# Kernel optimization log

Hardware: AMD Instinct MI355X
Metric: run time of the kernel (lower is better)

Reference implementation:

```python
import math
import jax, jax.numpy as jnp
import numpy as np

B, L, N, DM, H = 4, 12, 512, 64, 8
D = DM // H
FACTOR = 5  # args.spatial_factor


def setup_inputs() -> dict:
    key = jax.random.key(0)
    ks = jax.random.split(key, 6)
    s = 1.0 / math.sqrt(DM)
    return {
        "queries": jax.random.normal(ks[0], (B, L, N, DM), jnp.float32),
        "keys": jax.random.normal(ks[1], (B, L, N, DM), jnp.float32),
        "values": jax.random.normal(ks[2], (B, L, N, DM), jnp.float32),
        "Wq": jax.random.normal(ks[3], (DM, DM), jnp.float32) * s,
        "bq": jnp.zeros((DM,), jnp.float32),
        "Wk": jax.random.normal(ks[4], (DM, DM), jnp.float32) * s,
        "bk": jnp.zeros((DM,), jnp.float32),
        "Wv": jax.random.normal(ks[5], (DM, DM), jnp.float32) * s,
        "bv": jnp.zeros((DM,), jnp.float32),
    }


def reference(queries, keys, values, Wq, bq, Wk, bk, Wv, bv):
    # QKV projections (torch nn.Linear), then split heads and move to [B,H,N,L,D]
    q = jnp.transpose((queries @ Wq + bq).reshape(B, L, N, H, D), (0, 3, 2, 1, 4))
    k = jnp.transpose((keys @ Wk + bk).reshape(B, L, N, H, D), (0, 3, 2, 1, 4))
    v = jnp.transpose((values @ Wv + bv).reshape(B, L, N, H, D), (0, 3, 2, 1, 4))

    sample_k = min(FACTOR * int(np.ceil(np.log(N))), N)  # = n_top = effect_N

    # --- _prob_QK: random K sampling over the N (spatial) axis ---
    idx = jax.random.randint(jax.random.key(42), (N, sample_k), 0, N)  # [N, sk]
    K_sample = k[:, :, idx]                       # [B,H,N,sk,L,D] gather
    # Q.unsqueeze(-2) @ K_sample^T -> [B,H,N,L,sk], then transposed to [B,H,L,N,sk]
    qk_s = jnp.einsum('bhnld,bhnsld->bhlns', q, K_sample)
    M = qk_s.max(axis=-1) - qk_s.sum(axis=-1) / N  # sparsity measure [B,H,L,N]
    _, M_top = jax.lax.top_k(M, sample_k)          # [B,H,L,n_top]

    q_t = jnp.transpose(q, (0, 1, 3, 2, 4))        # [B,H,L,N,D]
    Q_red = jnp.take_along_axis(q_t, M_top[..., None], axis=3)  # [B,H,L,n_top,D]
    scores = jnp.einsum('bhltd,bhnld->bhltn', Q_red, k) / math.sqrt(D)

    # --- context: mean of V over nodes, overwritten at top queries ---
    attn = jax.nn.softmax(scores, axis=-1)                        # [B,H,L,n_top,N]
    attn_ret = jnp.einsum('bhltn,bhnld->bhltd', attn, v)          # [B,H,L,n_top,D]
    ctx = jnp.broadcast_to(v.mean(axis=2)[:, :, :, None, :], (B, H, L, N, D))
    bi = jnp.arange(B)[:, None, None, None]
    hi = jnp.arange(H)[None, :, None, None]
    li = jnp.arange(L)[None, None, :, None]
    ctx = ctx.at[bi, hi, li, M_top].set(attn_ret)                 # scatter-write

    out = jnp.transpose(ctx, (0, 2, 3, 1, 4)).reshape(B, L, N, DM)
    return out  # dropout p=0.0 -> identity
```

## Files before the change

kernel.cpp:

```cpp
#include <hip/hip_runtime.h>
#include <stdint.h>
#include <math.h>

#define BB 4
#define LL 12
#define NN 512
#define DMM 64
#define HH 8
#define DD 8
#define SK 35
#define IDX_TOTAL (NN*SK)
#define PADK 12

__device__ __forceinline__ void tf2x32(uint32_t k0, uint32_t k1, uint32_t x0, uint32_t x1,
                                       uint32_t& o0, uint32_t& o1) {
  const uint32_t ks2 = k0 ^ k1 ^ 0x1BD11BDAu;
  uint32_t a = x0 + k0, b = x1 + k1;
#define TF_R(r) { a += b; b = (b << (r)) | (b >> (32 - (r))); b ^= a; }
  TF_R(13) TF_R(15) TF_R(26) TF_R(6)
  a += k1;  b += ks2 + 1u;
  TF_R(17) TF_R(29) TF_R(16) TF_R(24)
  a += ks2; b += k0 + 2u;
  TF_R(13) TF_R(15) TF_R(26) TF_R(6)
  a += k0;  b += k1 + 3u;
  TF_R(17) TF_R(29) TF_R(16) TF_R(24)
  a += k1;  b += ks2 + 4u;
  TF_R(13) TF_R(15) TF_R(26) TF_R(6)
  a += ks2; b += k0 + 5u;
#undef TF_R
  o0 = a; o1 = b;
}

__global__ __launch_bounds__(256) void proj_idx_kernel(
    const float* __restrict__ Xq, const float* __restrict__ Xk, const float* __restrict__ Xv,
    const float* __restrict__ Wq_, const float* __restrict__ Wk_, const float* __restrict__ Wv_,
    const float* __restrict__ bq_, const float* __restrict__ bk_, const float* __restrict__ bv_,
    float* __restrict__ Oq, float* __restrict__ Ok, float* __restrict__ Ov,
    int* __restrict__ idxT) {
  const int tz = blockIdx.y;
  if (tz == 3) {
    int gid = blockIdx.x * 256 + threadIdx.x;
    if (gid < IDX_TOTAL) {
      int r = gid & (NN - 1);
      int s = gid >> 9;
      uint32_t ka, kb;
      tf2x32(0u, 42u, 0u, 1u, ka, kb);
      uint32_t b1, b2;
      tf2x32(ka, kb, 0u, (uint32_t)(r * SK + s), b1, b2);
      idxT[gid] = (int)((b1 ^ b2) & (uint32_t)(NN - 1));
    }
    return;
  }
  const float* X    = (tz == 0) ? Xq  : (tz == 1) ? Xk  : Xv;
  const float* W    = (tz == 0) ? Wq_ : (tz == 1) ? Wk_ : Wv_;
  const float* bias = (tz == 0) ? bq_ : (tz == 1) ? bk_ : bv_;
  float* O          = (tz == 0) ? Oq  : (tz == 1) ? Ok  : Ov;

  __shared__ __align__(16) float Ws[64][64];
  __shared__ __align__(16) float Xs[64][68];
  __shared__ float bs[64];

  const int tid = threadIdx.x;
  const size_t rowBase = (size_t)blockIdx.x * 64;
  const float* Xb = X + rowBase * 64;
  #pragma unroll
  for (int i = 0; i < 4; ++i) {
    int idx = tid + i*256;
    ((float4*)Ws)[idx] = ((const float4*)W)[idx];
    int r = idx >> 4, c = (idx & 15) << 2;
    *(float4*)&Xs[r][c] = ((const float4*)Xb)[idx];
  }
  if (tid < 64) bs[tid] = bias[tid];
  __syncthreads();

  const int hcol = tid & 7;
  const int rb   = tid >> 3;
  float4 bv0 = *(float4*)&bs[hcol*8];
  float4 bv1 = *(float4*)&bs[hcol*8+4];
  float acc[2][8];
  #pragma unroll
  for (int i = 0; i < 2; ++i) {
    acc[i][0]=bv0.x; acc[i][1]=bv0.y; acc[i][2]=bv0.z; acc[i][3]=bv0.w;
    acc[i][4]=bv1.x; acc[i][5]=bv1.y; acc[i][6]=bv1.z; acc[i][7]=bv1.w;
  }
  #pragma unroll 8
  for (int m = 0; m < 64; ++m) {
    float4 w0 = *(const float4*)&Ws[m][hcol*8];
    float4 w1 = *(const float4*)&Ws[m][hcol*8+4];
    float x0 = Xs[rb][m];
    float x1 = Xs[rb+32][m];
    acc[0][0]=fmaf(x0,w0.x,acc[0][0]); acc[0][1]=fmaf(x0,w0.y,acc[0][1]);
    acc[0][2]=fmaf(x0,w0.z,acc[0][2]); acc[0][3]=fmaf(x0,w0.w,acc[0][3]);
    acc[0][4]=fmaf(x0,w1.x,acc[0][4]); acc[0][5]=fmaf(x0,w1.y,acc[0][5]);
    acc[0][6]=fmaf(x0,w1.z,acc[0][6]); acc[0][7]=fmaf(x0,w1.w,acc[0][7]);
    acc[1][0]=fmaf(x1,w0.x,acc[1][0]); acc[1][1]=fmaf(x1,w0.y,acc[1][1]);
    acc[1][2]=fmaf(x1,w0.z,acc[1][2]); acc[1][3]=fmaf(x1,w0.w,acc[1][3]);
    acc[1][4]=fmaf(x1,w1.x,acc[1][4]); acc[1][5]=fmaf(x1,w1.y,acc[1][5]);
    acc[1][6]=fmaf(x1,w1.z,acc[1][6]); acc[1][7]=fmaf(x1,w1.w,acc[1][7]);
  }
  #pragma unroll
  for (int i = 0; i < 2; ++i) {
    size_t R = rowBase + rb + 32*i;
    int bI = (int)(R / (LL*NN));
    int lI = (int)((R / NN) % LL);
    int nI = (int)(R % NN);
    size_t off = ((((size_t)bI*HH + hcol)*LL + lI)*NN + nI)*DD;
    *(float4*)&O[off]     = make_float4(acc[i][0],acc[i][1],acc[i][2],acc[i][3]);
    *(float4*)&O[off + 4] = make_float4(acc[i][4],acc[i][5],acc[i][6],acc[i][7]);
  }
}

__global__ __launch_bounds__(256) void mkeys_kernel(
    const float* __restrict__ Qt, const float* __restrict__ Kt,
    const int* __restrict__ idxT, uint32_t* __restrict__ fkW) {
  const int gb = blockIdx.x;
  const int bid = gb >> 1, half = gb & 1;
  const int tid = threadIdx.x;
  __shared__ __align__(16) float Ks[NN][PADK];
  const size_t slabOff = (size_t)bid * (NN*DD);

  const float4* kg = (const float4*)(Kt + slabOff);
  #pragma unroll
  for (int i = 0; i < 2; ++i) {
    int r = tid + i*256;
    float4 a = kg[r*2], c = kg[r*2+1];
    *(float4*)&Ks[r][0] = a; *(float4*)&Ks[r][4] = c;
  }
  const int row = half*256 + tid;
  const float4* qp = (const float4*)(Qt + slabOff + (size_t)row*DD);
  float4 qa = qp[0], qb = qp[1];
  int jv[SK];
  const int* gi = idxT + row;
  #pragma unroll
  for (int s = 0; s < SK; ++s) jv[s] = gi[s*NN];
  __syncthreads();

  float mx = -INFINITY, sm = 0.f;
  #pragma unroll
  for (int s = 0; s < SK; ++s) {
    int j = jv[s];
    float4 c0 = *(const float4*)&Ks[j][0];
    float4 c1 = *(const float4*)&Ks[j][4];
    float dot = qa.x*c0.x + qa.y*c0.y + qa.z*c0.z + qa.w*c0.w
              + qb.x*c1.x + qb.y*c1.y + qb.z*c1.z + qb.w*c1.w;
    mx = fmaxf(mx, dot);
    sm += dot;
  }
  float m = mx - sm * (1.0f/NN);
  uint32_t u = __float_as_uint(m);
  fkW[bid*NN + row] = (u & 0x80000000u) ? ~u : (u | 0x80000000u);
}

__global__ __launch_bounds__(256) void attn2_kernel(
    const float* __restrict__ Qt, const float* __restrict__ Kt,
    const float* __restrict__ Vt, const uint32_t* __restrict__ fkW,
    float* __restrict__ out) {
  const int gb = blockIdx.x;
  const int bid = gb >> 1, half = gb & 1;
  const int l = bid % LL;
  const int h = (bid / LL) % HH;
  const int b = bid / (LL*HH);
  const int tid = threadIdx.x;
  const int wave = tid >> 6, lane = tid & 63;

  __shared__ __align__(16) uint64_t keys[NN];
  __shared__ int sel[256];
  __shared__ int listRow[SK];
  __shared__ int listSlot[SK];
  __shared__ int cnt2;
  __shared__ __align__(16) float attnOut[SK][8];
  __shared__ __align__(16) float redD[4][64][8];
  __shared__ __align__(16) float vm[8];

  const size_t slabOff = (size_t)bid * (NN*DD);

  {
    const uint32_t* fp = fkW + bid*NN;
    uint32_t f0 = fp[tid], f1 = fp[tid + 256];
    keys[tid]       = ((uint64_t)f0 << 32) | (uint32_t)(NN - 1 - tid);
    keys[tid + 256] = ((uint64_t)f1 << 32) | (uint32_t)(NN - 1 - (tid + 256));
  }
  sel[tid] = -1;
  if (tid == 0) cnt2 = 0;
  __syncthreads();

  {
    const int row = half*256 + tid;
    const uint64_t my = keys[row];
    const ulonglong2* kq = (const ulonglong2*)keys;
    int cnt = 0;
    #pragma unroll 8
    for (int jb = 0; jb < NN/2; ++jb) {
      ulonglong2 kv = kq[jb];
      cnt += (kv.x > my) ? 1 : 0;
      cnt += (kv.y > my) ? 1 : 0;
    }
    if (cnt < SK) {
      sel[tid] = cnt;
      int p = atomicAdd(&cnt2, 1);
      listRow[p] = row;
      listSlot[p] = cnt;
    }
  }
  __syncthreads();
  const int C = cnt2;

  const float4* kp = (const float4*)(Kt + slabOff);
  const float4* vp = (const float4*)(Vt + slabOff);

  if (wave == 0) {
    float a[8] = {0,0,0,0,0,0,0,0};
    #pragma unroll
    for (int j = 0; j < 8; ++j) {
      const float4* vr = vp + (size_t)(lane + 64*j)*2;
      float4 v0 = vr[0], v1 = vr[1];
      a[0]+=v0.x; a[1]+=v0.y; a[2]+=v0.z; a[3]+=v0.w;
      a[4]+=v1.x; a[5]+=v1.y; a[6]+=v1.z; a[7]+=v1.w;
    }
    *(float4*)&redD[0][lane][0] = make_float4(a[0],a[1],a[2],a[3]);
    *(float4*)&redD[0][lane][4] = make_float4(a[4],a[5],a[6],a[7]);
    const int d = lane & 7, g = lane >> 3;
    float s = 0.f;
    #pragma unroll
    for (int k = 0; k < 8; ++k) s += redD[0][g*8+k][d];
    s += __shfl_xor(s, 8); s += __shfl_xor(s, 16); s += __shfl_xor(s, 32);
    if (lane < 8) vm[lane] = s * (1.0f/NN);
  }

  auto do_rows = [&](int t1, int t2, bool has2) {
    const int n1 = listRow[t1];
    const int n2 = has2 ? listRow[t2] : n1;
    const int s1o = listSlot[t1];
    const int s2o = has2 ? listSlot[t2] : s1o;
    const float4* q1p = (const float4*)(Qt + slabOff + (size_t)n1*DD);
    const float4* q2p = (const float4*)(Qt + slabOff + (size_t)n2*DD);
    float4 q1a = q1p[0], q1b = q1p[1];
    float4 q2a = q2p[0], q2b = q2p[1];
    float p1[8], p2[8];
    float mx1 = -INFINITY, mx2 = -INFINITY;
    #pragma unroll
    for (int j = 0; j < 8; ++j) {
      int key = lane + 64*j;
      float4 ca = kp[key*2], cb = kp[key*2+1];
      float s1 = q1a.x*ca.x + q1a.y*ca.y + q1a.z*ca.z + q1a.w*ca.w
               + q1b.x*cb.x + q1b.y*cb.y + q1b.z*cb.z + q1b.w*cb.w;
      float s2 = q2a.x*ca.x + q2a.y*ca.y + q2a.z*ca.z + q2a.w*ca.w
               + q2b.x*cb.x + q2b.y*cb.y + q2b.z*cb.z + q2b.w*cb.w;
      s1 *= 0.35355339059327373f;
      s2 *= 0.35355339059327373f;
      p1[j] = s1; p2[j] = s2;
      mx1 = fmaxf(mx1, s1); mx2 = fmaxf(mx2, s2);
    }
    #pragma unroll
    for (int off = 32; off >= 1; off >>= 1) {
      mx1 = fmaxf(mx1, __shfl_xor(mx1, off));
      mx2 = fmaxf(mx2, __shfl_xor(mx2, off));
    }
    float sum1 = 0.f, sum2 = 0.f;
    #pragma unroll
    for (int j = 0; j < 8; ++j) {
      p1[j] = __expf(p1[j] - mx1); sum1 += p1[j];
      p2[j] = __expf(p2[j] - mx2); sum2 += p2[j];
    }
    #pragma unroll
    for (int off = 32; off >= 1; off >>= 1) {
      sum1 += __shfl_xor(sum1, off);
      sum2 += __shfl_xor(sum2, off);
    }
    float a1[8] = {0,0,0,0,0,0,0,0}, a2[8] = {0,0,0,0,0,0,0,0};
    #pragma unroll
    for (int j = 0; j < 8; ++j) {
      int key = lane + 64*j;
      float4 va = vp[key*2], vb = vp[key*2+1];
      float w1 = p1[j], w2 = p2[j];
      a1[0]=fmaf(w1,va.x,a1[0]); a1[1]=fmaf(w1,va.y,a1[1]);
      a1[2]=fmaf(w1,va.z,a1[2]); a1[3]=fmaf(w1,va.w,a1[3]);
      a1[4]=fmaf(w1,vb.x,a1[4]); a1[5]=fmaf(w1,vb.y,a1[5]);
      a1[6]=fmaf(w1,vb.z,a1[6]); a1[7]=fmaf(w1,vb.w,a1[7]);
      a2[0]=fmaf(w2,va.x,a2[0]); a2[1]=fmaf(w2,va.y,a2[1]);
      a2[2]=fmaf(w2,va.z,a2[2]); a2[3]=fmaf(w2,va.w,a2[3]);
      a2[4]=fmaf(w2,vb.x,a2[4]); a2[5]=fmaf(w2,vb.y,a2[5]);
      a2[6]=fmaf(w2,vb.z,a2[6]); a2[7]=fmaf(w2,vb.w,a2[7]);
    }
    const int d = lane & 7, g = lane >> 3;
    {
      *(float4*)&redD[wave][lane][0] = make_float4(a1[0],a1[1],a1[2],a1[3]);
      *(float4*)&redD[wave][lane][4] = make_float4(a1[4],a1[5],a1[6],a1[7]);
      float s = 0.f;
      #pragma unroll
      for (int k = 0; k < 8; ++k) s += redD[wave][g*8+k][d];
      s += __shfl_xor(s, 8); s += __shfl_xor(s, 16); s += __shfl_xor(s, 32);
      if (lane < 8) attnOut[s1o][lane] = s * (1.0f / sum1);
    }
    if (has2) {
      *(float4*)&redD[wave][lane][0] = make_float4(a2[0],a2[1],a2[2],a2[3]);
      *(float4*)&redD[wave][lane][4] = make_float4(a2[4],a2[5],a2[6],a2[7]);
      float s = 0.f;
      #pragma unroll
      for (int k = 0; k < 8; ++k) s += redD[wave][g*8+k][d];
      s += __shfl_xor(s, 8); s += __shfl_xor(s, 16); s += __shfl_xor(s, 32);
      if (lane < 8) attnOut[s2o][lane] = s * (1.0f / sum2);
    }
  };
  for (int it = wave*2; it < C; it += 8)
    do_rows(it, it + 1, (it + 1) < C);
  __syncthreads();

  {
    int t = sel[tid];
    float4 o0, o1;
    if (t >= 0) { o0 = *(const float4*)&attnOut[t][0]; o1 = *(const float4*)&attnOut[t][4]; }
    else        { o0 = *(const float4*)&vm[0];         o1 = *(const float4*)&vm[4]; }
    const int n = half*256 + tid;
    float* ob = out + ((size_t)(b*LL + l)*NN + n)*DMM + h*DD;
    *(float4*)&ob[0] = o0;
    *(float4*)&ob[4] = o1;
  }
}

extern "C" void kernel_launch(void* const* d_in, const int* in_sizes, int n_in,
                              void* d_out, int out_size, void* d_ws, size_t ws_size,
                              hipStream_t stream) {
  const float* q  = (const float*)d_in[0];
  const float* k  = (const float*)d_in[1];
  const float* v  = (const float*)d_in[2];
  const float* Wq = (const float*)d_in[3];
  const float* bq = (const float*)d_in[4];
  const float* Wk = (const float*)d_in[5];
  const float* bk = (const float*)d_in[6];
  const float* Wv = (const float*)d_in[7];
  const float* bv = (const float*)d_in[8];
  float* out = (float*)d_out;

  const size_t slab = (size_t)BB*HH*LL*NN*DD;
  float* qT = (float*)d_ws;
  float* kT = qT + slab;
  float* vT = kT + slab;
  int*   idxT = (int*)(vT + slab);
  uint32_t* fkW = (uint32_t*)(idxT + IDX_TOTAL);

  proj_idx_kernel<<<dim3((BB*LL*NN)/64, 4), 256, 0, stream>>>(
      q, k, v, Wq, Wk, Wv, bq, bk, bv, qT, kT, vT, idxT);
  mkeys_kernel<<<BB*HH*LL*2, 256, 0, stream>>>(qT, kT, idxT, fkW);
  attn2_kernel<<<BB*HH*LL*2, 256, 0, stream>>>(qT, kT, vT, fkW, out);
}
```

Measured before the change: 61.22 us.

## Fuse sparsity-measure kernel into attention kernel, keep K and Q in LDS

Merges the mkeys kernel into the attention kernel. Each block now computes the sparsity measure for all 512 rows from a shared-memory copy of K, instead of reading it from a global fkW buffer. The selected query rows are stashed in LDS, and the score pass reads K from LDS rather than global memory. This removes one kernel launch and the global round trip for fkW. In exchange, both half-blocks now do the full 512-row measure, doubling that work, and LDS use and register pressure go up.

```diff
diff --git a/kernel.cpp b/kernel.cpp
--- a/kernel.cpp
+++ b/kernel.cpp
@@ -110,50 +110,9 @@
   }
 }
 
-__global__ __launch_bounds__(256) void mkeys_kernel(
+__global__ __launch_bounds__(256) void back_kernel(
     const float* __restrict__ Qt, const float* __restrict__ Kt,
-    const int* __restrict__ idxT, uint32_t* __restrict__ fkW) {
-  const int gb = blockIdx.x;
-  const int bid = gb >> 1, half = gb & 1;
-  const int tid = threadIdx.x;
-  __shared__ __align__(16) float Ks[NN][PADK];
-  const size_t slabOff = (size_t)bid * (NN*DD);
-
-  const float4* kg = (const float4*)(Kt + slabOff);
-  #pragma unroll
-  for (int i = 0; i < 2; ++i) {
-    int r = tid + i*256;
-    float4 a = kg[r*2], c = kg[r*2+1];
-    *(float4*)&Ks[r][0] = a; *(float4*)&Ks[r][4] = c;
-  }
-  const int row = half*256 + tid;
-  const float4* qp = (const float4*)(Qt + slabOff + (size_t)row*DD);
-  float4 qa = qp[0], qb = qp[1];
-  int jv[SK];
-  const int* gi = idxT + row;
-  #pragma unroll
-  for (int s = 0; s < SK; ++s) jv[s] = gi[s*NN];
-  __syncthreads();
-
-  float mx = -INFINITY, sm = 0.f;
-  #pragma unroll
-  for (int s = 0; s < SK; ++s) {
-    int j = jv[s];
-    float4 c0 = *(const float4*)&Ks[j][0];
-    float4 c1 = *(const float4*)&Ks[j][4];
-    float dot = qa.x*c0.x + qa.y*c0.y + qa.z*c0.z + qa.w*c0.w
-              + qb.x*c1.x + qb.y*c1.y + qb.z*c1.z + qb.w*c1.w;
-    mx = fmaxf(mx, dot);
-    sm += dot;
-  }
-  float m = mx - sm * (1.0f/NN);
-  uint32_t u = __float_as_uint(m);
-  fkW[bid*NN + row] = (u & 0x80000000u) ? ~u : (u | 0x80000000u);
-}
-
-__global__ __launch_bounds__(256) void attn2_kernel(
-    const float* __restrict__ Qt, const float* __restrict__ Kt,
-    const float* __restrict__ Vt, const uint32_t* __restrict__ fkW,
+    const float* __restrict__ Vt, const int* __restrict__ idxT,
     float* __restrict__ out) {
   const int gb = blockIdx.x;
   const int bid = gb >> 1, half = gb & 1;
@@ -163,11 +122,13 @@
   const int tid = threadIdx.x;
   const int wave = tid >> 6, lane = tid & 63;
 
+  __shared__ __align__(16) float Ks[NN][PADK];
   __shared__ __align__(16) uint64_t keys[NN];
   __shared__ int sel[256];
   __shared__ int listRow[SK];
   __shared__ int listSlot[SK];
   __shared__ int cnt2;
+  __shared__ __align__(16) float Qw[SK][8];
   __shared__ __align__(16) float attnOut[SK][8];
   __shared__ __align__(16) float redD[4][64][8];
   __shared__ __align__(16) float vm[8];
@@ -175,13 +136,65 @@
   const size_t slabOff = (size_t)bid * (NN*DD);
 
   {
-    const uint32_t* fp = fkW + bid*NN;
-    uint32_t f0 = fp[tid], f1 = fp[tid + 256];
-    keys[tid]       = ((uint64_t)f0 << 32) | (uint32_t)(NN - 1 - tid);
-    keys[tid + 256] = ((uint64_t)f1 << 32) | (uint32_t)(NN - 1 - (tid + 256));
+    const float4* kg = (const float4*)(Kt + slabOff);
+    float4 a0 = kg[tid*2], a1 = kg[tid*2+1];
+    float4 b0 = kg[(tid+256)*2], b1 = kg[(tid+256)*2+1];
+    *(float4*)&Ks[tid][0] = a0;     *(float4*)&Ks[tid][4] = a1;
+    *(float4*)&Ks[tid+256][0] = b0; *(float4*)&Ks[tid+256][4] = b1;
+  }
+  const float4* qg = (const float4*)(Qt + slabOff);
+  float4 q0a = qg[tid*2],       q0b = qg[tid*2+1];
+  float4 q1a = qg[(tid+256)*2], q1b = qg[(tid+256)*2+1];
+  int jv1[SK];
+  {
+    const int* gi = idxT + tid;
+    #pragma unroll
+    for (int s = 0; s < SK; ++s) jv1[s] = gi[s*NN];
   }
   sel[tid] = -1;
   if (tid == 0) cnt2 = 0;
+  __syncthreads();
+
+  int jv2[SK];
+  {
+    const int* gi = idxT + tid + 256;
+    #pragma unroll
+    for (int s = 0; s < SK; ++s) jv2[s] = gi[s*NN];
+  }
+  {
+    float mx = -INFINITY, sm = 0.f;
+    #pragma unroll
+    for (int s = 0; s < SK; ++s) {
+      int j = jv1[s];
+      float4 c0 = *(const float4*)&Ks[j][0];
+      float4 c1 = *(const float4*)&Ks[j][4];
+      float dot = q0a.x*c0.x + q0a.y*c0.y + q0a.z*c0.z + q0a.w*c0.w
+                + q0b.x*c1.x + q0b.y*c1.y + q0b.z*c1.z + q0b.w*c1.w;
+      mx = fmaxf(mx, dot);
+      sm += dot;
+    }
+    float m = mx - sm * (1.0f/NN);
+    uint32_t u = __float_as_uint(m);
+    uint32_t fk = (u & 0x80000000u) ? ~u : (u | 0x80000000u);
+    keys[tid] = ((uint64_t)fk << 32) | (uint32_t)(NN - 1 - tid);
+  }
+  {
+    float mx = -INFINITY, sm = 0.f;
+    #pragma unroll
+    for (int s = 0; s < SK; ++s) {
+      int j = jv2[s];
+      float4 c0 = *(const float4*)&Ks[j][0];
+      float4 c1 = *(const float4*)&Ks[j][4];
+      float dot = q1a.x*c0.x + q1a.y*c0.y + q1a.z*c0.z + q1a.w*c0.w
+                + q1b.x*c1.x + q1b.y*c1.y + q1b.z*c1.z + q1b.w*c1.w;
+      mx = fmaxf(mx, dot);
+      sm += dot;
+    }
+    float m = mx - sm * (1.0f/NN);
+    uint32_t u = __float_as_uint(m);
+    uint32_t fk = (u & 0x80000000u) ? ~u : (u | 0x80000000u);
+    keys[tid + 256] = ((uint64_t)fk << 32) | (uint32_t)(NN - 1 - (tid + 256));
+  }
   __syncthreads();
 
   {
@@ -200,12 +213,15 @@
       int p = atomicAdd(&cnt2, 1);
       listRow[p] = row;
       listSlot[p] = cnt;
+      float4 mqa = half ? q1a : q0a;
+      float4 mqb = half ? q1b : q0b;
+      *(float4*)&Qw[p][0] = mqa;
+      *(float4*)&Qw[p][4] = mqb;
     }
   }
   __syncthreads();
   const int C = cnt2;
 
-  const float4* kp = (const float4*)(Kt + slabOff);
   const float4* vp = (const float4*)(Vt + slabOff);
 
   if (wave == 0) {
@@ -228,24 +244,23 @@
   }
 
   auto do_rows = [&](int t1, int t2, bool has2) {
-    const int n1 = listRow[t1];
-    const int n2 = has2 ? listRow[t2] : n1;
     const int s1o = listSlot[t1];
     const int s2o = has2 ? listSlot[t2] : s1o;
-    const float4* q1p = (const float4*)(Qt + slabOff + (size_t)n1*DD);
-    const float4* q2p = (const float4*)(Qt + slabOff + (size_t)n2*DD);
-    float4 q1a = q1p[0], q1b = q1p[1];
-    float4 q2a = q2p[0], q2b = q2p[1];
+    float4 q1aa = *(const float4*)&Qw[t1][0];
+    float4 q1bb = *(const float4*)&Qw[t1][4];
+    float4 q2aa = has2 ? *(const float4*)&Qw[t2][0] : q1aa;
+    float4 q2bb = has2 ? *(const float4*)&Qw[t2][4] : q1bb;
     float p1[8], p2[8];
     float mx1 = -INFINITY, mx2 = -INFINITY;
     #pragma unroll
     for (int j = 0; j < 8; ++j) {
       int key = lane + 64*j;
-      float4 ca = kp[key*2], cb = kp[key*2+1];
-      float s1 = q1a.x*ca.x + q1a.y*ca.y + q1a.z*ca.z + q1a.w*ca.w
-               + q1b.x*cb.x + q1b.y*cb.y + q1b.z*cb.z + q1b.w*cb.w;
-      float s2 = q2a.x*ca.x + q2a.y*ca.y + q2a.z*ca.z + q2a.w*ca.w
-               + q2b.x*cb.x + q2b.y*cb.y + q2b.z*cb.z + q2b.w*cb.w;
+      float4 ca = *(const float4*)&Ks[key][0];
+      float4 cb = *(const float4*)&Ks[key][4];
+      float s1 = q1aa.x*ca.x + q1aa.y*ca.y + q1aa.z*ca.z + q1aa.w*ca.w
+               + q1bb.x*cb.x + q1bb.y*cb.y + q1bb.z*cb.z + q1bb.w*cb.w;
+      float s2 = q2aa.x*ca.x + q2aa.y*ca.y + q2aa.z*ca.z + q2aa.w*ca.w
+               + q2bb.x*cb.x + q2bb.y*cb.y + q2bb.z*cb.z + q2bb.w*cb.w;
       s1 *= 0.35355339059327373f;
       s2 *= 0.35355339059327373f;
       p1[j] = s1; p2[j] = s2;
@@ -337,10 +352,8 @@
   float* kT = qT + slab;
   float* vT = kT + slab;
   int*   idxT = (int*)(vT + slab);
-  uint32_t* fkW = (uint32_t*)(idxT + IDX_TOTAL);
 
   proj_idx_kernel<<<dim3((BB*LL*NN)/64, 4), 256, 0, stream>>>(
       q, k, v, Wq, Wk, Wv, bq, bk, bv, qT, kT, vT, idxT);
-  mkeys_kernel<<<BB*HH*LL*2, 256, 0, stream>>>(qT, kT, idxT, fkW);
-  attn2_kernel<<<BB*HH*LL*2, 256, 0, stream>>>(qT, kT, vT, fkW, out);
+  back_kernel<<<BB*HH*LL*2, 256, 0, stream>>>(qT, kT, vT, idxT, out);
 }
```

Result: slower. 68.01 us (+11.1%).
